# Optimization experiments

Hardware: AMD Instinct MI355X
Metric: run time of the kernel (lower is better)

The kernel has to match this reference:

```python
import jax, jax.numpy as jnp
import numpy as np

V = 50000
E = 300000
B = 4
LAT = 512
H = 128
L = 3


def setup_inputs() -> dict:
    key = jax.random.key(0)
    ks = jax.random.split(key, 8)
    vertex_xyz = jax.random.normal(ks[0], (V, 3), jnp.float32)
    latent = jax.random.normal(ks[1], (B, LAT), jnp.float32)
    edge_index = jax.random.randint(ks[2], (2, E), 0, V, dtype=jnp.int32)
    def lin(k, out_f, in_f):
        return jax.random.normal(k, (out_f, in_f), jnp.float32) / np.float32(np.sqrt(in_f))
    W_in = lin(ks[3], H, LAT + 3)
    b_in = jnp.zeros((H,), jnp.float32)
    conv_W = jax.random.normal(ks[4], (L, H, H), jnp.float32) / np.float32(np.sqrt(H))
    conv_b = jnp.zeros((L, H), jnp.float32)
    W_out = lin(ks[5], 3, H)
    b_out = jnp.zeros((3,), jnp.float32)
    return dict(vertex_xyz=vertex_xyz, latent=latent, edge_index=edge_index,
                W_in=W_in, b_in=b_in, conv_W=conv_W, conv_b=conv_b,
                W_out=W_out, b_out=b_out)


def _edge_norm(edge_index, B_, V_):
    """GCN symmetric normalization for edge_index tiled B times (same node ids,
    as in the original code's edge_index.repeat(1, B)) plus self-loops on all
    N = B*V flattened nodes. Structure is identical across layers, so compute once."""
    N = B_ * V_
    ei = jnp.tile(edge_index, (1, B_))                 # (2, E*B), ids in [0, V)
    loops = jnp.arange(N, dtype=edge_index.dtype)
    row = jnp.concatenate([ei[0], loops])              # source
    col = jnp.concatenate([ei[1], loops])              # target
    deg = jax.ops.segment_sum(jnp.ones(row.shape, jnp.float32), col, num_segments=N)
    dis = jnp.where(deg > 0, jax.lax.rsqrt(jnp.maximum(deg, 1.0)), 0.0)
    norm = dis[row] * dis[col]                         # (E*B + N,)
    return row, col, norm, N


def reference(vertex_xyz, latent, edge_index, W_in, b_in, conv_W, conv_b, W_out, b_out):
    B_, V_ = latent.shape[0], vertex_xyz.shape[0]
    row, col, norm, N = _edge_norm(edge_index, B_, V_)

    # concat template xyz with broadcast latent -> (B*V, LAT+3)
    x = jnp.concatenate([
        jnp.broadcast_to(vertex_xyz[None], (B_, V_, 3)),
        jnp.broadcast_to(latent[:, None, :], (B_, V_, latent.shape[-1])),
    ], axis=-1).reshape(B_ * V_, -1)

    x = jax.nn.relu(x @ W_in.T + b_in)                 # (N, H)

    for l in range(conv_W.shape[0]):
        h = x @ conv_W[l].T                            # linear (no bias before aggregation)
        agg = jax.ops.segment_sum(norm[:, None] * h[row], col, num_segments=N)
        x = jax.nn.relu(agg + conv_b[l])

    out = x @ W_out.T + b_out                          # (N, 3)
    return out.reshape(B_, V_, 3)
```

## Files before the change

### kernel.cpp

```cpp
#include <hip/hip_runtime.h>
#include <hip/hip_bf16.h>

typedef __attribute__((ext_vector_type(8))) short short8;
typedef __attribute__((ext_vector_type(4))) float f32x4;

#define V_ 50000
#define E_ 300000
#define B_ 4
#define LAT_ 512
#define H_ 128
#define L_ 3
#define N_ (B_*V_)

#define SCAN_B 512
#define SCAN_G ((V_ + SCAN_B - 1) / SCAN_B)

__device__ inline void bsplit(float v, ushort& hi, ushort& lo) {
    __hip_bfloat16 hb = __float2bfloat16(v);
    float hf = __bfloat162float(hb);
    __hip_bfloat16 lb = __float2bfloat16(v - hf);
    hi = *(ushort*)&hb; lo = *(ushort*)&lb;
}


__global__ void k_zero(int* __restrict__ deg, int* __restrict__ cursor) {
    int i = blockIdx.x * 256 + threadIdx.x;
    if (i < V_) { deg[i] = 0; cursor[i] = 0; }
}

__global__ void k_deg(const int* __restrict__ dst, int* __restrict__ deg) {
    int e = blockIdx.x * 256 + threadIdx.x;
    if (e < E_) atomicAdd(&deg[dst[e]], 1);
}

__global__ __launch_bounds__(SCAN_B) void k_scan1(const int* __restrict__ deg,
                                                  int* __restrict__ off,
                                                  float* __restrict__ dis,
                                                  int* __restrict__ part) {
    int t = threadIdx.x;
    int i = blockIdx.x * SCAN_B + t;
    int d = (i < V_) ? deg[i] : 0;
    __shared__ int sm[SCAN_B];
    sm[t] = d;
    __syncthreads();
    int val = d;
    for (int s = 1; s < SCAN_B; s <<= 1) {
        int o = (t >= s) ? sm[t - s] : 0;
        __syncthreads();
        val += o;
        sm[t] = val;
        __syncthreads();
    }
    if (i < V_) {
        off[i] = val - d;
        dis[i] = rsqrtf((float)(B_ * d + 1));
    }
    if (t == SCAN_B - 1) part[blockIdx.x] = val;
}

__global__ void k_scan2(int* __restrict__ part) {
    __shared__ int sm[128];
    int t = threadIdx.x;
    int v = (t < SCAN_G) ? part[t] : 0;
    sm[t] = v;
    __syncthreads();
    int val = v;
    for (int s = 1; s < 128; s <<= 1) {
        int o = (t >= s) ? sm[t - s] : 0;
        __syncthreads();
        val += o;
        sm[t] = val;
        __syncthreads();
    }
    if (t < SCAN_G) part[t] = val - v;
}

__global__ __launch_bounds__(SCAN_B) void k_scan3(int* __restrict__ off,
                                                  const int* __restrict__ part) {
    int i = blockIdx.x * SCAN_B + threadIdx.x;
    if (i < V_) off[i] += part[blockIdx.x];
    if (i == 0) off[V_] = E_;
}

__global__ void k_fill(const int* __restrict__ src, const int* __restrict__ dst,
                       const int* __restrict__ off, int* __restrict__ cursor,
                       int* __restrict__ csr) {
    int e = blockIdx.x * 256 + threadIdx.x;
    if (e < E_) {
        int c = dst[e];
        int p = atomicAdd(&cursor[c], 1);
        csr[off[c] + p] = src[e];
    }
}


__global__ void k_wsplit(const float* __restrict__ W, ushort* __restrict__ Whi,
                         ushort* __restrict__ Wlo) {
    int i = blockIdx.x * 256 + threadIdx.x;
    float w = W[i];
    ushort hi, lo; bsplit(w, hi, lo);
    Whi[i] = hi; Wlo[i] = lo;
}

__global__ void k_prep(const float* __restrict__ Win, float* __restrict__ Wxyz) {
    int j = threadIdx.x;
    f32x4 v = {Win[(size_t)j*(LAT_+3)+0], Win[(size_t)j*(LAT_+3)+1],
               Win[(size_t)j*(LAT_+3)+2], 0.f};
    *(f32x4*)(Wxyz + j*4) = v;
}

__global__ void k_latproj(const float* __restrict__ Win, const float* __restrict__ bin,
                          const float* __restrict__ latent, float* __restrict__ latproj) {
    int t = blockIdx.x * 128 + threadIdx.x;
    if (t >= B_ * H_) return;
    int b = t >> 7, j = t & 127;
    const float* wr = Win + (size_t)j * (LAT_ + 3) + 3;
    const float* lp = latent + (size_t)b * LAT_;
    float s = bin[j];
    for (int k = 0; k < LAT_; k++) s = fmaf(wr[k], lp[k], s);
    latproj[t] = s;
}


__device__ inline void gemm_layer(const ushort* __restrict__ Ah,
                                  const ushort* __restrict__ Al,
                                  int l15, int kg,
                                  const short8 bh[4][2], const short8 bl[4][2],
                                  f32x4 acc[8][2]) {
#pragma unroll
    for (int m = 0; m < 8; m++) {
        const ushort* ph = Ah + (m*16 + l15)*H_ + kg*4;
        const ushort* pl = Al + (m*16 + l15)*H_ + kg*4;
        short8 ah[4], al[4];
#pragma unroll
        for (int ks = 0; ks < 4; ks++) {
            union { short8 v; uint2 u[2]; } uh, ul;
            uh.u[0] = *(const uint2*)(ph + ks*32);
            uh.u[1] = *(const uint2*)(ph + ks*32 + 16);
            ul.u[0] = *(const uint2*)(pl + ks*32);
            ul.u[1] = *(const uint2*)(pl + ks*32 + 16);
            ah[ks] = uh.v; al[ks] = ul.v;
        }
#pragma unroll
        for (int ks = 0; ks < 4; ks++)
#pragma unroll
            for (int nt = 0; nt < 2; nt++) {
                acc[m][nt] = __builtin_amdgcn_mfma_f32_16x16x32_bf16(ah[ks], bh[ks][nt], acc[m][nt], 0,0,0);
                acc[m][nt] = __builtin_amdgcn_mfma_f32_16x16x32_bf16(ah[ks], bl[ks][nt], acc[m][nt], 0,0,0);
                acc[m][nt] = __builtin_amdgcn_mfma_f32_16x16x32_bf16(al[ks], bh[ks][nt], acc[m][nt], 0,0,0);
            }
    }
}

__device__ inline void acc_to_bfrag(const f32x4 acc[8][2], const float* __restrict__ bias,
                                    int kg, short8 bh[4][2], short8 bl[4][2]) {
#pragma unroll
    for (int t = 0; t < 4; t++)
#pragma unroll
        for (int nt = 0; nt < 2; nt++) {
            union { short8 v; ushort s[8]; } uh, ul;
#pragma unroll
            for (int q = 0; q < 2; q++) {
                int m = 2*t + q;
                f32x4 b4 = *(const f32x4*)(bias + m*16 + kg*4);
#pragma unroll
                for (int j = 0; j < 4; j++) {
                    float s = fmaxf(acc[m][nt][j] + b4[j], 0.f);
                    bsplit(s, uh.s[q*4+j], ul.s[q*4+j]);
                }
            }
            bh[t][nt] = uh.v; bl[t][nt] = ul.v;
        }
}

__device__ inline void x0_bfrag(const float* __restrict__ xyz, const float* __restrict__ lp,
                                const float* __restrict__ Wxyz, int v, bool ok, int kg, int nt,
                                short8 bh[4][2], short8 bl[4][2]) {
    float x0 = xyz[v*3+0], x1 = xyz[v*3+1], x2 = xyz[v*3+2];
#pragma unroll
    for (int ks = 0; ks < 4; ks++) {
        union { short8 v; ushort s[8]; } uh, ul;
#pragma unroll
        for (int q = 0; q < 2; q++)
#pragma unroll
            for (int j = 0; j < 4; j++) {
                int f = ks*32 + q*16 + kg*4 + j;
                f32x4 wx = *(const f32x4*)(Wxyz + f*4);
                float s = lp[f];
                s = fmaf(wx[0], x0, s);
                s = fmaf(wx[1], x1, s);
                s = fmaf(wx[2], x2, s);
                s = fmaxf(s, 0.f);
                if (!ok) s = 0.f;
                bsplit(s, uh.s[q*4+j], ul.s[q*4+j]);
            }
        bh[ks][nt] = uh.v; bl[ks][nt] = ul.v;
    }
}


__global__ __launch_bounds__(256, 2) void k_big2(
        const float* __restrict__ xyz, const float* __restrict__ latproj,
        const float* __restrict__ Wxyz,
        const ushort* __restrict__ Whi, const ushort* __restrict__ Wlo,
        const float* __restrict__ convb,
        const float* __restrict__ Wout, const float* __restrict__ bout,
        float* __restrict__ out) {
    const int tid  = threadIdx.x;
    const int lane = tid & 63;
    const int l15  = lane & 15;
    const int kg   = lane >> 4;
    const int base = V_ + (blockIdx.x * 4 + (tid >> 6)) * 32;

    int node[2], vv[2]; bool ok[2];
    const float* lp[2];
#pragma unroll
    for (int nt = 0; nt < 2; nt++) {
        int n = base + nt*16 + l15;
        ok[nt] = (n < N_);
        int nn = ok[nt] ? n : 0;
        node[nt] = nn;
        int b = nn / V_;
        vv[nt] = nn - b * V_;
        lp[nt] = latproj + b * H_;
    }

    short8 bh[4][2], bl[4][2];
#pragma unroll
    for (int nt = 0; nt < 2; nt++)
        x0_bfrag(xyz, lp[nt], Wxyz, vv[nt], ok[nt], kg, nt, bh, bl);

    f32x4 acc[8][2];
    for (int l = 0; l < L_; l++) {
#pragma unroll
        for (int m = 0; m < 8; m++)
#pragma unroll
            for (int nt = 0; nt < 2; nt++) acc[m][nt] = (f32x4){0.f,0.f,0.f,0.f};
        gemm_layer(Whi + (size_t)l*H_*H_, Wlo + (size_t)l*H_*H_, l15, kg, bh, bl, acc);
        if (l < L_ - 1)
            acc_to_bfrag(acc, convb + l*H_, kg, bh, bl);
    }

    float p[2][3];
#pragma unroll
    for (int nt = 0; nt < 2; nt++) { p[nt][0] = 0.f; p[nt][1] = 0.f; p[nt][2] = 0.f; }
#pragma unroll
    for (int m = 0; m < 8; m++) {
        f32x4 b4 = *(const f32x4*)(convb + 2*H_ + m*16 + kg*4);
        f32x4 w0 = *(const f32x4*)(Wout + 0*H_ + m*16 + kg*4);
        f32x4 w1 = *(const f32x4*)(Wout + 1*H_ + m*16 + kg*4);
        f32x4 w2 = *(const f32x4*)(Wout + 2*H_ + m*16 + kg*4);
#pragma unroll
        for (int nt = 0; nt < 2; nt++)
#pragma unroll
            for (int j = 0; j < 4; j++) {
                float s = fmaxf(acc[m][nt][j] + b4[j], 0.f);
                p[nt][0] = fmaf(s, w0[j], p[nt][0]);
                p[nt][1] = fmaf(s, w1[j], p[nt][1]);
                p[nt][2] = fmaf(s, w2[j], p[nt][2]);
            }
    }
#pragma unroll
    for (int nt = 0; nt < 2; nt++)
#pragma unroll
        for (int o = 0; o < 3; o++) {
            p[nt][o] += __shfl_xor(p[nt][o], 16);
            p[nt][o] += __shfl_xor(p[nt][o], 32);
        }
    if (kg == 0) {
#pragma unroll
        for (int nt = 0; nt < 2; nt++)
            if (ok[nt]) {
                out[(size_t)node[nt]*3 + 0] = p[nt][0] + bout[0];
                out[(size_t)node[nt]*3 + 1] = p[nt][1] + bout[1];
                out[(size_t)node[nt]*3 + 2] = p[nt][2] + bout[2];
            }
    }
}


template<int MODE>
__global__ __launch_bounds__(256, 2) void k_lay0(
        const ushort* __restrict__ xh, const ushort* __restrict__ xl,
        const float* __restrict__ xyz, const float* __restrict__ latproj,
        const float* __restrict__ Wxyz,
        const ushort* __restrict__ Whp, const ushort* __restrict__ Wlp,
        float* __restrict__ h) {
    const int tid  = threadIdx.x;
    const int lane = tid & 63;
    const int l15  = lane & 15;
    const int kg   = lane >> 4;
    const int base = (blockIdx.x * 4 + (tid >> 6)) * 32;

    int node[2]; bool ok[2];
#pragma unroll
    for (int nt = 0; nt < 2; nt++) {
        int n = base + nt*16 + l15;
        ok[nt] = (n < V_);
        node[nt] = ok[nt] ? n : 0;
    }

    short8 bh[4][2], bl[4][2];
    if (MODE == 0) {
#pragma unroll
        for (int nt = 0; nt < 2; nt++)
            x0_bfrag(xyz, latproj, Wxyz, node[nt], ok[nt], kg, nt, bh, bl);
    } else {
#pragma unroll
        for (int nt = 0; nt < 2; nt++) {
            const ushort* ph = xh + (size_t)node[nt]*H_ + kg*4;
            const ushort* pl = xl + (size_t)node[nt]*H_ + kg*4;
#pragma unroll
            for (int ks = 0; ks < 4; ks++) {
                union { short8 v; uint2 u[2]; } uh, ul;
                uh.u[0] = *(const uint2*)(ph + ks*32);
                uh.u[1] = *(const uint2*)(ph + ks*32 + 16);
                ul.u[0] = *(const uint2*)(pl + ks*32);
                ul.u[1] = *(const uint2*)(pl + ks*32 + 16);
                bh[ks][nt] = uh.v; bl[ks][nt] = ul.v;
            }
        }
    }

    f32x4 acc[8][2];
#pragma unroll
    for (int m = 0; m < 8; m++)
#pragma unroll
        for (int nt = 0; nt < 2; nt++) acc[m][nt] = (f32x4){0.f,0.f,0.f,0.f};
    gemm_layer(Whp, Wlp, l15, kg, bh, bl, acc);

#pragma unroll
    for (int m = 0; m < 8; m++)
#pragma unroll
        for (int nt = 0; nt < 2; nt++)
            if (ok[nt])
                *(f32x4*)(h + (size_t)node[nt]*H_ + m*16 + kg*4) = acc[m][nt];
}


template<bool FINAL>
__global__ __launch_bounds__(256) void k_agg0(const float* __restrict__ h,
                                              const float* __restrict__ dis,
                                              const int* __restrict__ off,
                                              const int* __restrict__ csr,
                                              const float* __restrict__ bias,
                                              ushort* __restrict__ xh_out,
                                              ushort* __restrict__ xl_out,
                                              const float* __restrict__ Wout,
                                              const float* __restrict__ bout,
                                              float* __restrict__ out) {
    int c = blockIdx.x * 4 + (threadIdx.x >> 6);
    int lane = threadIdx.x & 63;
    if (c >= V_) return;
    int beg = off[c], end = off[c + 1];
    int nu = end - beg;
    int   myu  = (lane < nu) ? csr[beg + lane] : 0;
    float mywu = (lane < nu) ? dis[myu] : 0.f;
    float a0 = 0.f, a1 = 0.f;
    int nn = nu < 64 ? nu : 64;
    for (int i = 0; i < nn; i++) {
        int u = __shfl(myu, i);
        float wu = __shfl(mywu, i);
        const float* hu = h + (size_t)u * 128;
        a0 = fmaf(wu, hu[lane],      a0);
        a1 = fmaf(wu, hu[lane + 64], a1);
    }
    for (int i = beg + 64; i < end; i++) {
        int u = csr[i];
        float wu = dis[u];
        const float* hu = h + (size_t)u * 128;
        a0 = fmaf(wu, hu[lane],      a0);
        a1 = fmaf(wu, hu[lane + 64], a1);
    }
    float dc = dis[c];
    const float* hr = h + (size_t)c * 128;
    float s0 = fmaxf(dc * (float)B_ * a0 + dc * dc * hr[lane]      + bias[lane],      0.f);
    float s1 = fmaxf(dc * (float)B_ * a1 + dc * dc * hr[lane + 64] + bias[lane + 64], 0.f);
    if (FINAL) {
        float p0 = s0 * Wout[0*H_ + lane] + s1 * Wout[0*H_ + 64 + lane];
        float p1 = s0 * Wout[1*H_ + lane] + s1 * Wout[1*H_ + 64 + lane];
        float p2 = s0 * Wout[2*H_ + lane] + s1 * Wout[2*H_ + 64 + lane];
#pragma unroll
        for (int d = 32; d; d >>= 1) {
            p0 += __shfl_down(p0, d);
            p1 += __shfl_down(p1, d);
            p2 += __shfl_down(p2, d);
        }
        if (lane == 0) {
            out[(size_t)c*3 + 0] = p0 + bout[0];
            out[(size_t)c*3 + 1] = p1 + bout[1];
            out[(size_t)c*3 + 2] = p2 + bout[2];
        }
    } else {
        ushort h0, l0, h1, l1;
        bsplit(s0, h0, l0);
        bsplit(s1, h1, l1);
        xh_out[(size_t)c*128 + lane]      = h0;
        xl_out[(size_t)c*128 + lane]      = l0;
        xh_out[(size_t)c*128 + lane + 64] = h1;
        xl_out[(size_t)c*128 + lane + 64] = l1;
    }
}


extern "C" void kernel_launch(void* const* d_in, const int* in_sizes, int n_in,
                              void* d_out, int out_size, void* d_ws, size_t ws_size,
                              hipStream_t stream) {
    const float* xyz    = (const float*)d_in[0];
    const float* latent = (const float*)d_in[1];
    const int*   ei     = (const int*)d_in[2];
    const float* Win    = (const float*)d_in[3];
    const float* bin    = (const float*)d_in[4];
    const float* convW  = (const float*)d_in[5];
    const float* convb  = (const float*)d_in[6];
    const float* Wout   = (const float*)d_in[7];
    const float* bout   = (const float*)d_in[8];
    float* out = (float*)d_out;

    char* w = (char*)d_ws;
    auto carve = [&](size_t bytes) {
        char* p = w;
        w += (bytes + 255) & ~(size_t)255;
        return p;
    };
    ushort* xh      = (ushort*)carve((size_t)V_ * H_ * 2);
    ushort* xl      = (ushort*)carve((size_t)V_ * H_ * 2);
    float*  h       = (float*)carve((size_t)V_ * H_ * 4);
    ushort* Whi     = (ushort*)carve((size_t)L_ * H_ * H_ * 2);
    ushort* Wlo     = (ushort*)carve((size_t)L_ * H_ * H_ * 2);
    float*  dis     = (float*)carve((size_t)V_ * 4);
    float*  latproj = (float*)carve((size_t)B_ * H_ * 4);
    float*  Wxyz    = (float*)carve((size_t)H_ * 4 * 4);
    int*    deg     = (int*)carve((size_t)V_ * 4);
    int*    off     = (int*)carve((size_t)(V_ + 1) * 4);
    int*    cursor  = (int*)carve((size_t)V_ * 4);
    int*    csr     = (int*)carve((size_t)E_ * 4);
    int*    part    = (int*)carve((size_t)SCAN_G * 4);
    (void)ws_size; (void)in_sizes; (void)n_in; (void)out_size;

    const int* src = ei;
    const int* dst = ei + E_;

    k_zero<<<(V_ + 255) / 256, 256, 0, stream>>>(deg, cursor);
    k_deg<<<(E_ + 255) / 256, 256, 0, stream>>>(dst, deg);
    k_scan1<<<SCAN_G, SCAN_B, 0, stream>>>(deg, off, dis, part);
    k_scan2<<<1, 128, 0, stream>>>(part);
    k_scan3<<<SCAN_G, SCAN_B, 0, stream>>>(off, part);
    k_fill<<<(E_ + 255) / 256, 256, 0, stream>>>(src, dst, off, cursor, csr);

    k_wsplit<<<(L_ * H_ * H_) / 256, 256, 0, stream>>>(convW, Whi, Wlo);
    k_prep<<<1, 128, 0, stream>>>(Win, Wxyz);
    k_latproj<<<4, 128, 0, stream>>>(Win, bin, latent, latproj);

    const int GB = ((N_ - V_) + 127) / 128;
    k_big2<<<GB, 256, 0, stream>>>(xyz, latproj, Wxyz, Whi, Wlo,
                                   convb, Wout, bout, out);

    const int G0 = (V_ + 127) / 128;
    k_lay0<0><<<G0, 256, 0, stream>>>(nullptr, nullptr, xyz, latproj, Wxyz,
                                      Whi, Wlo, h);
    k_agg0<false><<<(V_ + 3) / 4, 256, 0, stream>>>(h, dis, off, csr, convb,
                                                    xh, xl, nullptr, nullptr, nullptr);
    k_lay0<1><<<G0, 256, 0, stream>>>(xh, xl, nullptr, nullptr, nullptr,
                                      Whi + (size_t)1*H_*H_, Wlo + (size_t)1*H_*H_, h);
    k_agg0<false><<<(V_ + 3) / 4, 256, 0, stream>>>(h, dis, off, csr, convb + 1*H_,
                                                    xh, xl, nullptr, nullptr, nullptr);
    k_lay0<1><<<G0, 256, 0, stream>>>(xh, xl, nullptr, nullptr, nullptr,
                                      Whi + (size_t)2*H_*H_, Wlo + (size_t)2*H_*H_, h);
    k_agg0<true><<<(V_ + 3) / 4, 256, 0, stream>>>(h, dis, off, csr, convb + 2*H_,
                                                   nullptr, nullptr, Wout, bout, out);
}
```

Baseline: 511.4 us.

## Replace fused register-resident MLP with persistent LDS-staged per-layer GEMM over all nodes

```diff
diff --git a/kernel.cpp b/kernel.cpp
--- a/kernel.cpp
+++ b/kernel.cpp
@@ -11,6 +11,7 @@
 #define H_ 128
 #define L_ 3
 #define N_ (B_*V_)
+#define NT_ (N_/64)
 
 #define SCAN_B 512
 #define SCAN_G ((V_ + SCAN_B - 1) / SCAN_B)
@@ -20,6 +21,17 @@
     float hf = __bfloat162float(hb);
     __hip_bfloat16 lb = __float2bfloat16(v - hf);
     hi = *(ushort*)&hb; lo = *(ushort*)&lb;
+}
+__device__ inline float bjoin(ushort h, ushort l) {
+    __hip_bfloat16 hb = *(__hip_bfloat16*)&h;
+    __hip_bfloat16 lb = *(__hip_bfloat16*)&l;
+    return __bfloat162float(hb) + __bfloat162float(lb);
+}
+
+__device__ inline void gload_lds16(const void* g, void* s) {
+    __builtin_amdgcn_global_load_lds(
+        (const __attribute__((address_space(1))) unsigned int*)g,
+        (__attribute__((address_space(3))) unsigned int*)s, 16, 0, 0);
 }
 
 
@@ -122,219 +134,139 @@
 }
 
 
-__device__ inline void gemm_layer(const ushort* __restrict__ Ah,
-                                  const ushort* __restrict__ Al,
-                                  int l15, int kg,
-                                  const short8 bh[4][2], const short8 bl[4][2],
-                                  f32x4 acc[8][2]) {
-#pragma unroll
-    for (int m = 0; m < 8; m++) {
-        const ushort* ph = Ah + (m*16 + l15)*H_ + kg*4;
-        const ushort* pl = Al + (m*16 + l15)*H_ + kg*4;
-        short8 ah[4], al[4];
-#pragma unroll
-        for (int ks = 0; ks < 4; ks++) {
-            union { short8 v; uint2 u[2]; } uh, ul;
-            uh.u[0] = *(const uint2*)(ph + ks*32);
-            uh.u[1] = *(const uint2*)(ph + ks*32 + 16);
-            ul.u[0] = *(const uint2*)(pl + ks*32);
-            ul.u[1] = *(const uint2*)(pl + ks*32 + 16);
-            ah[ks] = uh.v; al[ks] = ul.v;
-        }
-#pragma unroll
-        for (int ks = 0; ks < 4; ks++)
-#pragma unroll
-            for (int nt = 0; nt < 2; nt++) {
-                acc[m][nt] = __builtin_amdgcn_mfma_f32_16x16x32_bf16(ah[ks], bh[ks][nt], acc[m][nt], 0,0,0);
-                acc[m][nt] = __builtin_amdgcn_mfma_f32_16x16x32_bf16(ah[ks], bl[ks][nt], acc[m][nt], 0,0,0);
-                acc[m][nt] = __builtin_amdgcn_mfma_f32_16x16x32_bf16(al[ks], bh[ks][nt], acc[m][nt], 0,0,0);
-            }
-    }
-}
-
-__device__ inline void acc_to_bfrag(const f32x4 acc[8][2], const float* __restrict__ bias,
-                                    int kg, short8 bh[4][2], short8 bl[4][2]) {
-#pragma unroll
-    for (int t = 0; t < 4; t++)
-#pragma unroll
-        for (int nt = 0; nt < 2; nt++) {
-            union { short8 v; ushort s[8]; } uh, ul;
-#pragma unroll
-            for (int q = 0; q < 2; q++) {
-                int m = 2*t + q;
-                f32x4 b4 = *(const f32x4*)(bias + m*16 + kg*4);
-#pragma unroll
-                for (int j = 0; j < 4; j++) {
-                    float s = fmaxf(acc[m][nt][j] + b4[j], 0.f);
-                    bsplit(s, uh.s[q*4+j], ul.s[q*4+j]);
-                }
-            }
-            bh[t][nt] = uh.v; bl[t][nt] = ul.v;
-        }
-}
-
-__device__ inline void x0_bfrag(const float* __restrict__ xyz, const float* __restrict__ lp,
-                                const float* __restrict__ Wxyz, int v, bool ok, int kg, int nt,
-                                short8 bh[4][2], short8 bl[4][2]) {
+__global__ __launch_bounds__(256) void k_x0(const float* __restrict__ xyz,
+                                            const float* __restrict__ latproj,
+                                            const float* __restrict__ Wxyz,
+                                            ushort* __restrict__ xh,
+                                            ushort* __restrict__ xl) {
+    int idx = blockIdx.x * 256 + threadIdx.x;
+    int node = idx >> 4;
+    int c0 = (idx & 15) * 8;
+    int b = node / V_, v = node - b * V_;
     float x0 = xyz[v*3+0], x1 = xyz[v*3+1], x2 = xyz[v*3+2];
-#pragma unroll
-    for (int ks = 0; ks < 4; ks++) {
-        union { short8 v; ushort s[8]; } uh, ul;
-#pragma unroll
-        for (int q = 0; q < 2; q++)
-#pragma unroll
-            for (int j = 0; j < 4; j++) {
-                int f = ks*32 + q*16 + kg*4 + j;
-                f32x4 wx = *(const f32x4*)(Wxyz + f*4);
-                float s = lp[f];
-                s = fmaf(wx[0], x0, s);
-                s = fmaf(wx[1], x1, s);
-                s = fmaf(wx[2], x2, s);
-                s = fmaxf(s, 0.f);
-                if (!ok) s = 0.f;
-                bsplit(s, uh.s[q*4+j], ul.s[q*4+j]);
-            }
-        bh[ks][nt] = uh.v; bl[ks][nt] = ul.v;
-    }
-}
-
-
-__global__ __launch_bounds__(256, 2) void k_big2(
-        const float* __restrict__ xyz, const float* __restrict__ latproj,
-        const float* __restrict__ Wxyz,
-        const ushort* __restrict__ Whi, const ushort* __restrict__ Wlo,
-        const float* __restrict__ convb,
-        const float* __restrict__ Wout, const float* __restrict__ bout,
-        float* __restrict__ out) {
+    ushort hs[8], ls[8];
+#pragma unroll
+    for (int i = 0; i < 8; i++) {
+        int f = c0 + i;
+        f32x4 wx = *(const f32x4*)(Wxyz + f*4);
+        float s = latproj[b*H_ + f];
+        s = fmaf(wx[0], x0, s);
+        s = fmaf(wx[1], x1, s);
+        s = fmaf(wx[2], x2, s);
+        s = fmaxf(s, 0.f);
+        bsplit(s, hs[i], ls[i]);
+    }
+    *(uint4*)(xh + (size_t)node*H_ + c0) = *(uint4*)hs;
+    *(uint4*)(xl + (size_t)node*H_ + c0) = *(uint4*)ls;
+}
+
+
+__global__ __launch_bounds__(512, 2) void k_layer(
+        const ushort* __restrict__ xh, const ushort* __restrict__ xl,
+        const ushort* __restrict__ Wh, const ushort* __restrict__ Wl,
+        const float* __restrict__ bias,
+        float* __restrict__ h,
+        ushort* __restrict__ xho, ushort* __restrict__ xlo) {
+    __shared__ __align__(16) char smem[65536];
     const int tid  = threadIdx.x;
+    const int w    = tid >> 6;
     const int lane = tid & 63;
     const int l15  = lane & 15;
     const int kg   = lane >> 4;
-    const int base = V_ + (blockIdx.x * 4 + (tid >> 6)) * 32;
-
-    int node[2], vv[2]; bool ok[2];
-    const float* lp[2];
-#pragma unroll
-    for (int nt = 0; nt < 2; nt++) {
-        int n = base + nt*16 + l15;
-        ok[nt] = (n < N_);
-        int nn = ok[nt] ? n : 0;
-        node[nt] = nn;
-        int b = nn / V_;
-        vv[nt] = nn - b * V_;
-        lp[nt] = latproj + b * H_;
-    }
-
-    short8 bh[4][2], bl[4][2];
+    const int n0   = (w & 3) * 32;
+    const int mrow = (w >> 2) * 32;
+
+    short8 wh[2][4], wl[2][4];
 #pragma unroll
     for (int nt = 0; nt < 2; nt++)
-        x0_bfrag(xyz, lp[nt], Wxyz, vv[nt], ok[nt], kg, nt, bh, bl);
-
-    f32x4 acc[8][2];
-    for (int l = 0; l < L_; l++) {
-#pragma unroll
-        for (int m = 0; m < 8; m++)
-#pragma unroll
-            for (int nt = 0; nt < 2; nt++) acc[m][nt] = (f32x4){0.f,0.f,0.f,0.f};
-        gemm_layer(Whi + (size_t)l*H_*H_, Wlo + (size_t)l*H_*H_, l15, kg, bh, bl, acc);
-        if (l < L_ - 1)
-            acc_to_bfrag(acc, convb + l*H_, kg, bh, bl);
-    }
-
-    float p[2][3];
-#pragma unroll
-    for (int nt = 0; nt < 2; nt++) { p[nt][0] = 0.f; p[nt][1] = 0.f; p[nt][2] = 0.f; }
-#pragma unroll
-    for (int m = 0; m < 8; m++) {
-        f32x4 b4 = *(const f32x4*)(convb + 2*H_ + m*16 + kg*4);
-        f32x4 w0 = *(const f32x4*)(Wout + 0*H_ + m*16 + kg*4);
-        f32x4 w1 = *(const f32x4*)(Wout + 1*H_ + m*16 + kg*4);
-        f32x4 w2 = *(const f32x4*)(Wout + 2*H_ + m*16 + kg*4);
-#pragma unroll
-        for (int nt = 0; nt < 2; nt++)
-#pragma unroll
-            for (int j = 0; j < 4; j++) {
-                float s = fmaxf(acc[m][nt][j] + b4[j], 0.f);
-                p[nt][0] = fmaf(s, w0[j], p[nt][0]);
-                p[nt][1] = fmaf(s, w1[j], p[nt][1]);
-                p[nt][2] = fmaf(s, w2[j], p[nt][2]);
+#pragma unroll
+        for (int ks = 0; ks < 4; ks++) {
+            const ushort* bh = Wh + (size_t)(n0 + nt*16 + l15)*H_ + ks*32 + kg*4;
+            const ushort* bl = Wl + (size_t)(n0 + nt*16 + l15)*H_ + ks*32 + kg*4;
+            union { short8 v; uint2 u[2]; } uh, ul;
+            uh.u[0] = *(const uint2*)bh;  uh.u[1] = *(const uint2*)(bh + 16);
+            ul.u[0] = *(const uint2*)bl;  ul.u[1] = *(const uint2*)(bl + 16);
+            wh[nt][ks] = uh.v; wl[nt][ks] = ul.v;
+        }
+
+    const float bv[2] = { bias[n0 + l15], bias[n0 + 16 + l15] };
+
+    const int srow = w * 8;
+    const int rgl  = lane >> 4;
+    const int cch  = lane & 15;
+    auto stage = [&](int tile, int bufoff) {
+#pragma unroll
+        for (int i = 0; i < 4; i++) {
+            int p  = i >> 1, rg = i & 1;
+            int row = srow + rg*4 + rgl;
+            int node = tile*64 + row;
+            const ushort* src = (p ? xl : xh) + (size_t)node*H_ + ((cch ^ (row & 7)) << 3);
+            char* dst = smem + bufoff + p*16384 + (srow + rg*4)*256;
+            gload_lds16(src, dst);
+        }
+    };
+
+    int tile = blockIdx.x;
+    stage(tile, 0);
+    __syncthreads();
+    int buf = 0;
+
+    for (; tile < NT_; tile += gridDim.x) {
+        int nxt = tile + gridDim.x;
+        if (nxt < NT_) stage(nxt, (buf ^ 1) * 32768);
+
+        const char* sb = smem + buf * 32768;
+        f32x4 acc[2][2];
+        acc[0][0] = acc[0][1] = acc[1][0] = acc[1][1] = (f32x4){0.f,0.f,0.f,0.f};
+        const int r7 = l15 & 7;
+#pragma unroll
+        for (int ks = 0; ks < 4; ks++) {
+            short8 ah[2], al[2];
+            const int cl = (((ks*4 + (kg>>1)) ^ r7) << 4) + (kg & 1) * 8;
+            const int ch = (((ks*4 + (kg>>1) + 2) ^ r7) << 4) + (kg & 1) * 8;
+#pragma unroll
+            for (int mt = 0; mt < 2; mt++) {
+                const char* rb = sb + (mrow + mt*16 + l15) * 256;
+                union { short8 v; uint2 u[2]; } uh, ul;
+                uh.u[0] = *(const uint2*)(rb + cl);
+                uh.u[1] = *(const uint2*)(rb + ch);
+                ul.u[0] = *(const uint2*)(rb + 16384 + cl);
+                ul.u[1] = *(const uint2*)(rb + 16384 + ch);
+                ah[mt] = uh.v; al[mt] = ul.v;
             }
-    }
-#pragma unroll
-    for (int nt = 0; nt < 2; nt++)
-#pragma unroll
-        for (int o = 0; o < 3; o++) {
-            p[nt][o] += __shfl_xor(p[nt][o], 16);
-            p[nt][o] += __shfl_xor(p[nt][o], 32);
+#pragma unroll
+            for (int mt = 0; mt < 2; mt++)
+#pragma unroll
+                for (int nt = 0; nt < 2; nt++) {
+                    acc[mt][nt] = __builtin_amdgcn_mfma_f32_16x16x32_bf16(ah[mt], wh[nt][ks], acc[mt][nt], 0,0,0);
+                    acc[mt][nt] = __builtin_amdgcn_mfma_f32_16x16x32_bf16(al[mt], wh[nt][ks], acc[mt][nt], 0,0,0);
+                    acc[mt][nt] = __builtin_amdgcn_mfma_f32_16x16x32_bf16(ah[mt], wl[nt][ks], acc[mt][nt], 0,0,0);
+                }
         }
-    if (kg == 0) {
-#pragma unroll
-        for (int nt = 0; nt < 2; nt++)
-            if (ok[nt]) {
-                out[(size_t)node[nt]*3 + 0] = p[nt][0] + bout[0];
-                out[(size_t)node[nt]*3 + 1] = p[nt][1] + bout[1];
-                out[(size_t)node[nt]*3 + 2] = p[nt][2] + bout[2];
+
+        const int tbase = tile * 64 + mrow;
+#pragma unroll
+        for (int mt = 0; mt < 2; mt++)
+#pragma unroll
+            for (int nt = 0; nt < 2; nt++) {
+                const int col = n0 + nt*16 + l15;
+#pragma unroll
+                for (int j = 0; j < 4; j++) {
+                    int node = tbase + mt*16 + kg*4 + j;
+                    float v = acc[mt][nt][j];
+                    if (node < V_) {
+                        h[(size_t)node*H_ + col] = v;
+                    } else {
+                        float s = fmaxf(v + bv[nt], 0.f);
+                        ushort hi, lo; bsplit(s, hi, lo);
+                        xho[(size_t)node*H_ + col] = hi;
+                        xlo[(size_t)node*H_ + col] = lo;
+                    }
+                }
             }
-    }
-}
-
-
-template<int MODE>
-__global__ __launch_bounds__(256, 2) void k_lay0(
-        const ushort* __restrict__ xh, const ushort* __restrict__ xl,
-        const float* __restrict__ xyz, const float* __restrict__ latproj,
-        const float* __restrict__ Wxyz,
-        const ushort* __restrict__ Whp, const ushort* __restrict__ Wlp,
-        float* __restrict__ h) {
-    const int tid  = threadIdx.x;
-    const int lane = tid & 63;
-    const int l15  = lane & 15;
-    const int kg   = lane >> 4;
-    const int base = (blockIdx.x * 4 + (tid >> 6)) * 32;
-
-    int node[2]; bool ok[2];
-#pragma unroll
-    for (int nt = 0; nt < 2; nt++) {
-        int n = base + nt*16 + l15;
-        ok[nt] = (n < V_);
-        node[nt] = ok[nt] ? n : 0;
-    }
-
-    short8 bh[4][2], bl[4][2];
-    if (MODE == 0) {
-#pragma unroll
-        for (int nt = 0; nt < 2; nt++)
-            x0_bfrag(xyz, latproj, Wxyz, node[nt], ok[nt], kg, nt, bh, bl);
-    } else {
-#pragma unroll
-        for (int nt = 0; nt < 2; nt++) {
-            const ushort* ph = xh + (size_t)node[nt]*H_ + kg*4;
-            const ushort* pl = xl + (size_t)node[nt]*H_ + kg*4;
-#pragma unroll
-            for (int ks = 0; ks < 4; ks++) {
-                union { short8 v; uint2 u[2]; } uh, ul;
-                uh.u[0] = *(const uint2*)(ph + ks*32);
-                uh.u[1] = *(const uint2*)(ph + ks*32 + 16);
-                ul.u[0] = *(const uint2*)(pl + ks*32);
-                ul.u[1] = *(const uint2*)(pl + ks*32 + 16);
-                bh[ks][nt] = uh.v; bl[ks][nt] = ul.v;
-            }
-        }
-    }
-
-    f32x4 acc[8][2];
-#pragma unroll
-    for (int m = 0; m < 8; m++)
-#pragma unroll
-        for (int nt = 0; nt < 2; nt++) acc[m][nt] = (f32x4){0.f,0.f,0.f,0.f};
-    gemm_layer(Whp, Wlp, l15, kg, bh, bl, acc);
-
-#pragma unroll
-    for (int m = 0; m < 8; m++)
-#pragma unroll
-        for (int nt = 0; nt < 2; nt++)
-            if (ok[nt])
-                *(f32x4*)(h + (size_t)node[nt]*H_ + m*16 + kg*4) = acc[m][nt];
+        __syncthreads();
+        buf ^= 1;
+    }
 }
 
 
@@ -403,6 +335,29 @@
 }
 
 
+__global__ __launch_bounds__(256) void k_out(const ushort* __restrict__ xh,
+                                             const ushort* __restrict__ xl,
+                                             const float* __restrict__ Wout,
+                                             const float* __restrict__ bout,
+                                             float* __restrict__ out) {
+    int n = V_ + (int)(((size_t)blockIdx.x * 256 + threadIdx.x) >> 6);
+    int lane = threadIdx.x & 63;
+    if (n >= N_) return;
+    const ushort* ph = xh + (size_t)n * 128;
+    const ushort* pl = xl + (size_t)n * 128;
+    ushort u0h = ph[lane], u0l = pl[lane], u1h = ph[lane + 64], u1l = pl[lane + 64];
+    float x0 = bjoin(u0h, u0l);
+    float x1 = bjoin(u1h, u1l);
+#pragma unroll
+    for (int o = 0; o < 3; o++) {
+        float a = x0 * Wout[o * 128 + lane] + x1 * Wout[o * 128 + 64 + lane];
+#pragma unroll
+        for (int d = 32; d; d >>= 1) a += __shfl_down(a, d);
+        if (lane == 0) out[(size_t)n * 3 + o] = a + bout[o];
+    }
+}
+
+
 extern "C" void kernel_launch(void* const* d_in, const int* in_sizes, int n_in,
                               void* d_out, int out_size, void* d_ws, size_t ws_size,
                               hipStream_t stream) {
@@ -423,8 +378,8 @@
         w += (bytes + 255) & ~(size_t)255;
         return p;
     };
-    ushort* xh      = (ushort*)carve((size_t)V_ * H_ * 2);
-    ushort* xl      = (ushort*)carve((size_t)V_ * H_ * 2);
+    ushort* xh      = (ushort*)carve((size_t)N_ * H_ * 2);
+    ushort* xl      = (ushort*)carve((size_t)N_ * H_ * 2);
     float*  h       = (float*)carve((size_t)V_ * H_ * 4);
     ushort* Whi     = (ushort*)carve((size_t)L_ * H_ * H_ * 2);
     ushort* Wlo     = (ushort*)carve((size_t)L_ * H_ * H_ * 2);
@@ -452,21 +407,23 @@
     k_prep<<<1, 128, 0, stream>>>(Win, Wxyz);
     k_latproj<<<4, 128, 0, stream>>>(Win, bin, latent, latproj);
 
-    const int GB = ((N_ - V_) + 127) / 128;
-    k_big2<<<GB, 256, 0, stream>>>(xyz, latproj, Wxyz, Whi, Wlo,
-                                   convb, Wout, bout, out);
-
-    const int G0 = (V_ + 127) / 128;
-    k_lay0<0><<<G0, 256, 0, stream>>>(nullptr, nullptr, xyz, latproj, Wxyz,
-                                      Whi, Wlo, h);
-    k_agg0<false><<<(V_ + 3) / 4, 256, 0, stream>>>(h, dis, off, csr, convb,
-                                                    xh, xl, nullptr, nullptr, nullptr);
-    k_lay0<1><<<G0, 256, 0, stream>>>(xh, xl, nullptr, nullptr, nullptr,
-                                      Whi + (size_t)1*H_*H_, Wlo + (size_t)1*H_*H_, h);
-    k_agg0<false><<<(V_ + 3) / 4, 256, 0, stream>>>(h, dis, off, csr, convb + 1*H_,
-                                                    xh, xl, nullptr, nullptr, nullptr);
-    k_lay0<1><<<G0, 256, 0, stream>>>(xh, xl, nullptr, nullptr, nullptr,
-                                      Whi + (size_t)2*H_*H_, Wlo + (size_t)2*H_*H_, h);
-    k_agg0<true><<<(V_ + 3) / 4, 256, 0, stream>>>(h, dis, off, csr, convb + 2*H_,
-                                                   nullptr, nullptr, Wout, bout, out);
-}
+    k_x0<<<(N_ * 16) / 256, 256, 0, stream>>>(xyz, latproj, Wxyz, xh, xl);
+
+    for (int l = 0; l < L_; l++) {
+        k_layer<<<512, 512, 0, stream>>>(xh, xl,
+                                         Whi + (size_t)l * H_ * H_,
+                                         Wlo + (size_t)l * H_ * H_,
+                                         convb + (size_t)l * H_,
+                                         h, xh, xl);
+        if (l < L_ - 1)
+            k_agg0<false><<<(V_ + 3) / 4, 256, 0, stream>>>(h, dis, off, csr,
+                                                            convb + (size_t)l * H_,
+                                                            xh, xl, nullptr, nullptr, nullptr);
+        else
+            k_agg0<true><<<(V_ + 3) / 4, 256, 0, stream>>>(h, dis, off, csr,
+                                                           convb + (size_t)l * H_,
+                                                           nullptr, nullptr, Wout, bout, out);
+    }
+
+    k_out<<<(N_ - V_) / 4, 256, 0, stream>>>(xh, xl, Wout, bout, out);
+}
```

After: 429.0 us. 16.1% less time.
